# Performance work log

Measured on AMD Instinct MI355X. Metric: run time of the kernel, lower is better.

## Reference

```python
import math
import jax, jax.numpy as jnp
import numpy as np

B = 8          # number of graphs in the batch
NMAX = 256     # max nodes per graph (padding size)
K = 128        # num_kernels
H = 32         # num_heads
NTYPE = 101    # max_node_type + 1


def setup_inputs() -> dict:
    key = jax.random.key(0)
    ks = jax.random.split(key, 10)
    sizes = np.asarray(NMAX - np.arange(B) * 16, dtype=np.int32)  # 256,240,...,144 -> ragged
    N = int(sizes.sum())  # 1600
    coord = jax.random.normal(ks[0], (N, 3), dtype=jnp.float32) * 3.0
    node_type = jax.random.randint(ks[1], (N,), 0, NTYPE, dtype=jnp.int32)
    gaussian_means = jax.random.uniform(ks[2], (1, K), minval=0.0, maxval=3.0, dtype=jnp.float32)
    gaussian_stds = jax.random.uniform(ks[3], (1, K), minval=0.0, maxval=3.0, dtype=jnp.float32)
    # nn.Embedding(max_node_type+1, 2) tables; original init is const(0)/const(1),
    # we perturb so the computation is non-degenerate.
    mul_w = jax.random.normal(ks[4], (NTYPE, 2), dtype=jnp.float32) * 0.1
    bias_w = 1.0 + jax.random.normal(ks[5], (NTYPE, 2), dtype=jnp.float32) * 0.1
    W1 = jax.random.normal(ks[6], (K, K), dtype=jnp.float32) / math.sqrt(K)
    b1 = jnp.zeros((K,), dtype=jnp.float32)
    W2 = jax.random.normal(ks[7], (K, H), dtype=jnp.float32) / math.sqrt(K)
    b2 = jnp.zeros((H,), dtype=jnp.float32)
    return {
        "coord": coord,
        "gaussian_means": gaussian_means,
        "gaussian_stds": gaussian_stds,
        "mul_w": mul_w,
        "bias_w": bias_w,
        "W1": W1,
        "b1": b1,
        "W2": W2,
        "b2": b2,
        "node_type": node_type,
        "batch_num_nodes": jnp.asarray(sizes),
    }


def reference(coord, gaussian_means, gaussian_stds, mul_w, bias_w, W1, b1, W2, b2,
              node_type, batch_num_nodes):
    N = coord.shape[0]
    offsets = jnp.concatenate([jnp.zeros((1,), dtype=batch_num_nodes.dtype),
                               jnp.cumsum(batch_num_nodes)[:-1]])
    ar = jnp.arange(NMAX)
    idx = offsets[:, None] + ar[None, :]                     # [B, n] flat node index per graph slot
    valid = ar[None, :] < batch_num_nodes[:, None]           # [B, n] node mask
    idx_c = jnp.clip(idx, 0, N - 1)
    pc = coord[idx_c]                                        # [B, n, 3] padded coords
    pt = node_type[idx_c]                                    # [B, n]

    # pairwise Euclidean distance (torch.cdist p=2), sqrt-safe at 0
    diff = pc[:, :, None, :] - pc[:, None, :, :]             # [B, n, n, 3]
    sq = jnp.sum(diff * diff, axis=-1)                       # [B, n, n]
    nz = sq > 0
    dist = jnp.where(nz, jnp.sqrt(jnp.where(nz, sq, 1.0)), 0.0)

    # outer-sum of per-node (src, dst) scaling embeddings
    mul_e = mul_w[pt]                                        # [B, n, 2]
    bias_e = bias_w[pt]
    mul = mul_e[:, :, None, 0] + mul_e[:, None, :, 1]        # [B, n, n]
    bias = bias_e[:, :, None, 0] + bias_e[:, None, :, 1]
    scaled = mul * dist + bias                               # [B, n, n]

    means = gaussian_means.reshape(-1)                       # [K]
    stds = jnp.abs(gaussian_stds.reshape(-1)) + 0.01         # [K]
    z = (scaled[..., None] - means) / stds                   # [B, n, n, K]
    gk = jnp.exp(-0.5 * z * z) / (-math.sqrt(2.0 * math.pi) * stds)

    h = jax.nn.gelu(gk @ W1 + b1, approximate=False)         # exact gelu like torch F.gelu
    out = h @ W2 + b2                                        # [B, n, n, H]

    pair = valid[:, :, None] & valid[:, None, :]             # padded positions -> -inf
    return jnp.where(pair[..., None], out, -jnp.inf)
```

## Files before the change

### kernel.cpp

```cpp
#include <hip/hip_runtime.h>
#include <math.h>

#define NMAXC 256
#define KC 128
#define HC 32
#define BC 8
#define TP 256
#define NEG_SENTINEL (-1.0e30f)
#define LOG2E 1.4426950408889634f

typedef __bf16 bf16x8 __attribute__((ext_vector_type(8)));
typedef float  f32x16 __attribute__((ext_vector_type(16)));
union FragU { uint4 u; bf16x8 v; };

#if __has_builtin(__builtin_amdgcn_exp2f)
#define EXP2F(x) __builtin_amdgcn_exp2f(x)
#else
#define EXP2F(x) exp2f(x)
#endif

__device__ __forceinline__ unsigned pack2(float lo, float hi) {
    return __builtin_amdgcn_perm(__float_as_uint(hi), __float_as_uint(lo), 0x07060302u);
}

__device__ __forceinline__ int swap23(int k) {
    return (k & ~12) | ((k & 4) << 1) | ((k & 8) >> 1);
}

__global__ __launch_bounds__(256) void se3d_prep(const float* __restrict__ W1,
                                                 const float* __restrict__ W2,
                                                 const float* __restrict__ gm,
                                                 const float* __restrict__ gs,
                                                 const int* __restrict__ bnn,
                                                 unsigned* __restrict__ wsu) {
    int t = blockIdx.x * 256 + threadIdx.x;
    if (t < 2048) {
        int fb = t >> 6, lane = t & 63;
        int nt = fb >> 3, ks = fb & 7;
        int n  = nt * 32 + (lane & 31);
        int k0 = ks * 16 + 8 * (lane >> 5);
        unsigned u[4];
#pragma unroll
        for (int p = 0; p < 4; ++p)
            u[p] = pack2(-W1[(k0 + 2 * p) * KC + n], -W1[(k0 + 2 * p + 1) * KC + n]);
        ((uint4*)wsu)[t] = make_uint4(u[0], u[1], u[2], u[3]);
    } else if (t < 2560) {
        int c = t - 2048;
        int ks = c >> 6, lane = c & 63;
        int n  = lane & 31;
        int k0 = ks * 16 + 8 * (lane >> 5);
        unsigned u[4];
#pragma unroll
        for (int p = 0; p < 4; ++p) {
            int ta = swap23(k0 + 2 * p);
            int tb = swap23(k0 + 2 * p + 1);
            u[p] = pack2(W2[ta * HC + n], W2[tb * HC + n]);
        }
        ((uint4*)wsu)[2048 + c] = make_uint4(u[0], u[1], u[2], u[3]);
    } else if (t < 2688) {
        int k = t - 2560;
        float inv = 1.0f / (fabsf(gs[k]) + 0.01f);
        float m  = gm[k];
        float A2 = -0.5f * inv * inv * LOG2E;
        float* wf = (float*)wsu + 10240;
        wf[2 * k]     = A2;
        wf[2 * k + 1] = -2.0f * A2 * m;
        wf[256 + k]   = A2 * m * m + log2f(0.3989422804014327f * inv);
    } else if (t < 2696) {
        int g = t - 2688;
        int o = 0;
        for (int i = 0; i < g; ++i) o += bnn[i];
        ((int*)wsu)[10624 + g] = o;
    } else if (t < 2704) {
        int g = t - 2696;
        unsigned n = (unsigned)bnn[g];
        wsu[10632 + g] = (1u << 25) / n + 1u;
    }
}

__global__ __launch_bounds__(256, 3) void se3d_main(
    const float* __restrict__ coord, const float* __restrict__ mulw,
    const float* __restrict__ biasw, const float* __restrict__ b1,
    const float* __restrict__ b2, const int* __restrict__ ntype,
    const int* __restrict__ bnn, const void* __restrict__ ws,
    float* __restrict__ out)
{
    __shared__ __attribute__((aligned(16))) uint4 ldsW[2560];
    __shared__ float scaled[TP];
    __shared__ int   obase[TP];
    __shared__ float cAB[2 * KC];
    __shared__ float cC[KC];

    const int b = blockIdx.y;
    const int n = bnn[b];
    const int q0 = blockIdx.x * TP;
    const int tid = threadIdx.x;

    if (q0 >= n * n) {
        int v = q0 + tid - n * n;
        int wdt = 256 - n;
        int na = n * wdt;
        int i, j;
        if (v < na) { i = v / wdt; j = n + (v - i * wdt); }
        else        { int vp = v - na; i = n + (vp >> 8); j = vp & 255; }
        float4 s4 = make_float4(NEG_SENTINEL, NEG_SENTINEL, NEG_SENTINEL, NEG_SENTINEL);
        float4* o = (float4*)(out + ((size_t)((b * NMAXC + i) * NMAXC + j)) * HC);
#pragma unroll
        for (int t = 0; t < 8; ++t) o[t] = s4;
        return;
    }

    const int l = tid & 63, w = tid >> 6;

#pragma unroll
    for (int t = 0; t < 10; ++t) {
        int chunk = w * 10 + t;
        __builtin_amdgcn_global_load_lds(
            (const uint4*)ws + chunk * 64 + l,
            &ldsW[chunk * 64], 16, 0, 0);
    }

    const int      off = ((const int*)ws)[10624 + b];
    const unsigned mg  = ((const unsigned*)ws)[10632 + b];

    const float* wf = (const float*)((const char*)ws + 40960);
    cAB[tid < 256 ? tid : 0] = wf[tid < 256 ? tid : 0];
    if (tid < KC) cC[tid] = wf[256 + tid];
    {
        int q = q0 + tid;
        int i = (int)(((unsigned long long)(unsigned)q * mg) >> 25);
        int j = q - i * n;
        int gi = off + i, gj = off + j;
        float dx = coord[gi * 3 + 0] - coord[gj * 3 + 0];
        float dy = coord[gi * 3 + 1] - coord[gj * 3 + 1];
        float dz = coord[gi * 3 + 2] - coord[gj * 3 + 2];
        float sq = dx * dx + dy * dy + dz * dz;
        float dist = sq > 0.f ? sqrtf(sq) : 0.f;
        int ti = ntype[gi], tj = ntype[gj];
        scaled[tid] = (mulw[ti * 2 + 0] + mulw[tj * 2 + 1]) * dist
                    + (biasw[ti * 2 + 0] + biasw[tj * 2 + 1]);
        obase[tid]  = ((b * NMAXC + i) * NMAXC + j) * HC;
    }
    __syncthreads();

    const int hi = l >> 5, ln31 = l & 31;
    const int m0 = w * 64;
    const float sA = scaled[m0 + ln31];
    const float sB = scaled[m0 + 32 + ln31];

    const bf16x8* wsW1 = (const bf16x8*)ldsW;
    const bf16x8* wsW2 = (const bf16x8*)ldsW + 2048;

    FragU gfrA[8], gfrB[8];
#pragma unroll
    for (int ks = 0; ks < 8; ++ks) {
        int k0 = ks * 16 + 8 * hi;
        const float4* ab = (const float4*)(cAB + 2 * k0);
        const float4* cc = (const float4*)(cC + k0);
        float4 ab0 = ab[0], ab1 = ab[1], ab2 = ab[2], ab3 = ab[3];
        float4 c0 = cc[0], c1 = cc[1];
#pragma unroll
        for (int grp = 0; grp < 2; ++grp) {
            float s = grp ? sB : sA;
            float t0 = EXP2F(fmaf(fmaf(ab0.x, s, ab0.y), s, c0.x));
            float t1 = EXP2F(fmaf(fmaf(ab0.z, s, ab0.w), s, c0.y));
            float t2 = EXP2F(fmaf(fmaf(ab1.x, s, ab1.y), s, c0.z));
            float t3 = EXP2F(fmaf(fmaf(ab1.z, s, ab1.w), s, c0.w));
            float t4 = EXP2F(fmaf(fmaf(ab2.x, s, ab2.y), s, c1.x));
            float t5 = EXP2F(fmaf(fmaf(ab2.z, s, ab2.w), s, c1.y));
            float t6 = EXP2F(fmaf(fmaf(ab3.x, s, ab3.y), s, c1.z));
            float t7 = EXP2F(fmaf(fmaf(ab3.z, s, ab3.w), s, c1.w));
            FragU& g = grp ? gfrB[ks] : gfrA[ks];
            g.u.x = pack2(t0, t1);
            g.u.y = pack2(t2, t3);
            g.u.z = pack2(t4, t5);
            g.u.w = pack2(t6, t7);
        }
    }

    const float KSG = -1.702f * LOG2E;
    f32x16 c2A, c2B;
#pragma unroll
    for (int g = 0; g < 4; ++g) {
        float4 t4 = *(const float4*)(b2 + 8 * g + 4 * hi);
        c2A[4 * g + 0] = t4.x; c2A[4 * g + 1] = t4.y;
        c2A[4 * g + 2] = t4.z; c2A[4 * g + 3] = t4.w;
        c2B[4 * g + 0] = t4.x; c2B[4 * g + 1] = t4.y;
        c2B[4 * g + 2] = t4.z; c2B[4 * g + 3] = t4.w;
    }

#define GELU_PACK(AA, F0, F1) do {                                      \
    float vv[16];                                                       \
    _Pragma("unroll")                                                   \
    for (int r = 0; r < 16; ++r) {                                      \
        float x = AA[r];                                                \
        float e = EXP2F(x * KSG);                                       \
        vv[r] = x * __builtin_amdgcn_rcpf(1.0f + e);                    \
    }                                                                   \
    F0.u.x = pack2(vv[0],  vv[1]);  F0.u.y = pack2(vv[2],  vv[3]);      \
    F0.u.z = pack2(vv[4],  vv[5]);  F0.u.w = pack2(vv[6],  vv[7]);      \
    F1.u.x = pack2(vv[8],  vv[9]);  F1.u.y = pack2(vv[10], vv[11]);     \
    F1.u.z = pack2(vv[12], vv[13]); F1.u.w = pack2(vv[14], vv[15]);     \
} while (0)

#pragma unroll
    for (int nt = 0; nt < 4; ++nt) {
        f32x16 aA, aB;
#pragma unroll
        for (int g = 0; g < 4; ++g) {
            float4 t4 = *(const float4*)(b1 + nt * 32 + 8 * g + 4 * hi);
            aA[4 * g + 0] = t4.x; aA[4 * g + 1] = t4.y;
            aA[4 * g + 2] = t4.z; aA[4 * g + 3] = t4.w;
            aB[4 * g + 0] = t4.x; aB[4 * g + 1] = t4.y;
            aB[4 * g + 2] = t4.z; aB[4 * g + 3] = t4.w;
        }
#pragma unroll
        for (int ks = 0; ks < 8; ++ks) {
            bf16x8 w0 = wsW1[(nt * 8 + ks) * 64 + l];
            aA = __builtin_amdgcn_mfma_f32_32x32x16_bf16(w0, gfrA[ks].v, aA, 0, 0, 0);
            aB = __builtin_amdgcn_mfma_f32_32x32x16_bf16(w0, gfrB[ks].v, aB, 0, 0, 0);
        }
        FragU fA0, fA1, fB0, fB1;
        GELU_PACK(aA, fA0, fA1);
        GELU_PACK(aB, fB0, fB1);
        bf16x8 u0 = wsW2[(2 * nt + 0) * 64 + l];
        bf16x8 u1 = wsW2[(2 * nt + 1) * 64 + l];
        c2A = __builtin_amdgcn_mfma_f32_32x32x16_bf16(u0, fA0.v, c2A, 0, 0, 0);
        c2A = __builtin_amdgcn_mfma_f32_32x32x16_bf16(u1, fA1.v, c2A, 0, 0, 0);
        c2B = __builtin_amdgcn_mfma_f32_32x32x16_bf16(u0, fB0.v, c2B, 0, 0, 0);
        c2B = __builtin_amdgcn_mfma_f32_32x32x16_bf16(u1, fB1.v, c2B, 0, 0, 0);
    }
#undef GELU_PACK

    {
        const int obA = obase[m0 + ln31];
        float* opA = out + (size_t)obA + 4 * hi;
#pragma unroll
        for (int g = 0; g < 4; ++g)
            *(float4*)(opA + 8 * g) =
                make_float4(c2A[4 * g], c2A[4 * g + 1], c2A[4 * g + 2], c2A[4 * g + 3]);
        const int obB = obase[m0 + 32 + ln31];
        float* opB = out + (size_t)obB + 4 * hi;
#pragma unroll
        for (int g = 0; g < 4; ++g)
            *(float4*)(opB + 8 * g) =
                make_float4(c2B[4 * g], c2B[4 * g + 1], c2B[4 * g + 2], c2B[4 * g + 3]);
    }
}

extern "C" void kernel_launch(void* const* d_in, const int* in_sizes, int n_in,
                              void* d_out, int out_size, void* d_ws, size_t ws_size,
                              hipStream_t stream) {
    const float* coord = (const float*)d_in[0];
    const float* gm    = (const float*)d_in[1];
    const float* gs    = (const float*)d_in[2];
    const float* mulw  = (const float*)d_in[3];
    const float* biasw = (const float*)d_in[4];
    const float* W1    = (const float*)d_in[5];
    const float* b1    = (const float*)d_in[6];
    const float* W2    = (const float*)d_in[7];
    const float* b2    = (const float*)d_in[8];
    const int* ntype   = (const int*)d_in[9];
    const int* bnn     = (const int*)d_in[10];
    float* out = (float*)d_out;

    hipLaunchKernelGGL(se3d_prep, dim3(11), dim3(256), 0, stream,
                       W1, W2, gm, gs, bnn, (unsigned*)d_ws);
    hipLaunchKernelGGL(se3d_main, dim3(NMAXC * NMAXC / TP, BC), dim3(256),
                       0, stream,
                       coord, mulw, biasw, b1, b2, ntype, bnn, d_ws, out);
}
```

Before: 117.2 us.

## Make main kernel persistent with prefetched per-tile pair setup

```diff
diff --git a/kernel.cpp b/kernel.cpp
--- a/kernel.cpp
+++ b/kernel.cpp
@@ -6,6 +6,8 @@
 #define HC 32
 #define BC 8
 #define TP 256
+#define NTILES 2048
+#define PBLK 768
 #define NEG_SENTINEL (-1.0e30f)
 #define LOG2E 1.4426950408889634f
 
@@ -75,6 +77,8 @@
         int g = t - 2696;
         unsigned n = (unsigned)bnn[g];
         wsu[10632 + g] = (1u << 25) / n + 1u;
+    } else {
+        wsu[10640 + (t - 2704)] = 0u;
     }
 }
 
@@ -85,167 +89,193 @@
     const int* __restrict__ bnn, const void* __restrict__ ws,
     float* __restrict__ out)
 {
-    __shared__ __attribute__((aligned(16))) uint4 ldsW[2560];
-    __shared__ float scaled[TP];
-    __shared__ int   obase[TP];
-    __shared__ float cAB[2 * KC];
-    __shared__ float cC[KC];
-
-    const int b = blockIdx.y;
-    const int n = bnn[b];
-    const int q0 = blockIdx.x * TP;
+    __shared__ __attribute__((aligned(16))) uint4 ldsW[2688];
+    __shared__ float scaled[2][TP];
+    __shared__ int   obase[2][TP];
+
     const int tid = threadIdx.x;
-
-    if (q0 >= n * n) {
-        int v = q0 + tid - n * n;
-        int wdt = 256 - n;
-        int na = n * wdt;
-        int i, j;
-        if (v < na) { i = v / wdt; j = n + (v - i * wdt); }
-        else        { int vp = v - na; i = n + (vp >> 8); j = vp & 255; }
-        float4 s4 = make_float4(NEG_SENTINEL, NEG_SENTINEL, NEG_SENTINEL, NEG_SENTINEL);
-        float4* o = (float4*)(out + ((size_t)((b * NMAXC + i) * NMAXC + j)) * HC);
-#pragma unroll
-        for (int t = 0; t < 8; ++t) o[t] = s4;
-        return;
-    }
-
     const int l = tid & 63, w = tid >> 6;
-
-#pragma unroll
-    for (int t = 0; t < 10; ++t) {
-        int chunk = w * 10 + t;
-        __builtin_amdgcn_global_load_lds(
-            (const uint4*)ws + chunk * 64 + l,
-            &ldsW[chunk * 64], 16, 0, 0);
-    }
-
-    const int      off = ((const int*)ws)[10624 + b];
-    const unsigned mg  = ((const unsigned*)ws)[10632 + b];
-
-    const float* wf = (const float*)((const char*)ws + 40960);
-    cAB[tid < 256 ? tid : 0] = wf[tid < 256 ? tid : 0];
-    if (tid < KC) cC[tid] = wf[256 + tid];
-    {
-        int q = q0 + tid;
-        int i = (int)(((unsigned long long)(unsigned)q * mg) >> 25);
-        int j = q - i * n;
-        int gi = off + i, gj = off + j;
-        float dx = coord[gi * 3 + 0] - coord[gj * 3 + 0];
-        float dy = coord[gi * 3 + 1] - coord[gj * 3 + 1];
-        float dz = coord[gi * 3 + 2] - coord[gj * 3 + 2];
-        float sq = dx * dx + dy * dy + dz * dz;
-        float dist = sq > 0.f ? sqrtf(sq) : 0.f;
-        int ti = ntype[gi], tj = ntype[gj];
-        scaled[tid] = (mulw[ti * 2 + 0] + mulw[tj * 2 + 1]) * dist
-                    + (biasw[ti * 2 + 0] + biasw[tj * 2 + 1]);
-        obase[tid]  = ((b * NMAXC + i) * NMAXC + j) * HC;
-    }
-    __syncthreads();
-
     const int hi = l >> 5, ln31 = l & 31;
     const int m0 = w * 64;
-    const float sA = scaled[m0 + ln31];
-    const float sB = scaled[m0 + 32 + ln31];
-
-    const bf16x8* wsW1 = (const bf16x8*)ldsW;
-    const bf16x8* wsW2 = (const bf16x8*)ldsW + 2048;
-
-    FragU gfrA[8], gfrB[8];
-#pragma unroll
-    for (int ks = 0; ks < 8; ++ks) {
-        int k0 = ks * 16 + 8 * hi;
-        const float4* ab = (const float4*)(cAB + 2 * k0);
-        const float4* cc = (const float4*)(cC + k0);
-        float4 ab0 = ab[0], ab1 = ab[1], ab2 = ab[2], ab3 = ab[3];
-        float4 c0 = cc[0], c1 = cc[1];
-#pragma unroll
-        for (int grp = 0; grp < 2; ++grp) {
-            float s = grp ? sB : sA;
-            float t0 = EXP2F(fmaf(fmaf(ab0.x, s, ab0.y), s, c0.x));
-            float t1 = EXP2F(fmaf(fmaf(ab0.z, s, ab0.w), s, c0.y));
-            float t2 = EXP2F(fmaf(fmaf(ab1.x, s, ab1.y), s, c0.z));
-            float t3 = EXP2F(fmaf(fmaf(ab1.z, s, ab1.w), s, c0.w));
-            float t4 = EXP2F(fmaf(fmaf(ab2.x, s, ab2.y), s, c1.x));
-            float t5 = EXP2F(fmaf(fmaf(ab2.z, s, ab2.w), s, c1.y));
-            float t6 = EXP2F(fmaf(fmaf(ab3.x, s, ab3.y), s, c1.z));
-            float t7 = EXP2F(fmaf(fmaf(ab3.z, s, ab3.w), s, c1.w));
-            FragU& g = grp ? gfrB[ks] : gfrA[ks];
-            g.u.x = pack2(t0, t1);
-            g.u.y = pack2(t2, t3);
-            g.u.z = pack2(t4, t5);
-            g.u.w = pack2(t6, t7);
+
+    {
+        int nch  = 11 - (w >> 1);
+        int base = (w < 2) ? (w * 11) : (22 + (w - 2) * 10);
+        for (int t = 0; t < nch; ++t) {
+            int chunk = base + t;
+            __builtin_amdgcn_global_load_lds(
+                (const uint4*)ws + chunk * 64 + l,
+                &ldsW[chunk * 64], 16, 0, 0);
         }
     }
 
-    const float KSG = -1.702f * LOG2E;
-    f32x16 c2A, c2B;
-#pragma unroll
-    for (int g = 0; g < 4; ++g) {
-        float4 t4 = *(const float4*)(b2 + 8 * g + 4 * hi);
-        c2A[4 * g + 0] = t4.x; c2A[4 * g + 1] = t4.y;
-        c2A[4 * g + 2] = t4.z; c2A[4 * g + 3] = t4.w;
-        c2B[4 * g + 0] = t4.x; c2B[4 * g + 1] = t4.y;
-        c2B[4 * g + 2] = t4.z; c2B[4 * g + 3] = t4.w;
+#define SETUP(T, SV, OBV, TV) do {                                          \
+    int bb_ = (T) >> 8;                                                     \
+    int nn_ = bnn[bb_];                                                     \
+    int qq0_ = ((T) & 255) * TP;                                            \
+    (TV) = qq0_ < nn_ * nn_;                                                \
+    if (TV) {                                                               \
+        int off_      = ((const int*)ws)[10624 + bb_];                      \
+        unsigned mg_  = ((const unsigned*)ws)[10632 + bb_];                 \
+        int q_ = qq0_ + tid;                                                \
+        int i_ = (int)(((unsigned long long)(unsigned)q_ * mg_) >> 25);     \
+        int j_ = q_ - i_ * nn_;                                             \
+        int gi_ = off_ + i_, gj_ = off_ + j_;                               \
+        float dx_ = coord[gi_*3+0] - coord[gj_*3+0];                        \
+        float dy_ = coord[gi_*3+1] - coord[gj_*3+1];                        \
+        float dz_ = coord[gi_*3+2] - coord[gj_*3+2];                        \
+        float sq_ = dx_*dx_ + dy_*dy_ + dz_*dz_;                            \
+        float dist_ = sq_ > 0.f ? sqrtf(sq_) : 0.f;                         \
+        int ti_ = ntype[gi_], tj_ = ntype[gj_];                             \
+        (SV) = (mulw[ti_*2+0] + mulw[tj_*2+1]) * dist_                      \
+             + (biasw[ti_*2+0] + biasw[tj_*2+1]);                           \
+        (OBV) = ((bb_ * NMAXC + i_) * NMAXC + j_) * HC;                     \
+    }                                                                       \
+} while (0)
+
+    int T = blockIdx.x;
+    int cur = 0;
+    {
+        float sv; int obv; bool tv;
+        SETUP(T, sv, obv, tv);
+        if (tv) { scaled[0][tid] = sv; obase[0][tid] = obv; }
+        bool curval = tv;
+        __syncthreads();
+
+        const bf16x8* wsW1 = (const bf16x8*)ldsW;
+        const bf16x8* wsW2 = (const bf16x8*)ldsW + 2048;
+        const float*  wfAB = (const float*)ldsW + 10240;
+        const float*  wfC  = wfAB + 256;
+        const float KSG = -1.702f * LOG2E;
+
+        while (true) {
+            int Tn = T + PBLK;
+            bool have_next = Tn < NTILES;
+            float sv2; int obv2; bool tv2 = false;
+            if (have_next) SETUP(Tn, sv2, obv2, tv2);
+
+            if (!curval) {
+                int bb = T >> 8;
+                int nn = bnn[bb];
+                int qq0 = (T & 255) * TP;
+                int v = qq0 + tid - nn * nn;
+                int wdt = 256 - nn;
+                int na = nn * wdt;
+                int i, j;
+                if (v < na) { i = v / wdt; j = nn + (v - i * wdt); }
+                else        { int vp = v - na; i = nn + (vp >> 8); j = vp & 255; }
+                float4 s4 = make_float4(NEG_SENTINEL, NEG_SENTINEL,
+                                        NEG_SENTINEL, NEG_SENTINEL);
+                float4* o = (float4*)(out + ((size_t)((bb * NMAXC + i) * NMAXC + j)) * HC);
+#pragma unroll
+                for (int t = 0; t < 8; ++t) o[t] = s4;
+            } else {
+                const float sA = scaled[cur][m0 + ln31];
+                const float sB = scaled[cur][m0 + 32 + ln31];
+
+                FragU gfrA[8], gfrB[8];
+#pragma unroll
+                for (int ks = 0; ks < 8; ++ks) {
+                    int k0 = ks * 16 + 8 * hi;
+                    const float4* ab = (const float4*)(wfAB + 2 * k0);
+                    const float4* cc = (const float4*)(wfC + k0);
+                    float4 ab0 = ab[0], ab1 = ab[1], ab2 = ab[2], ab3 = ab[3];
+                    float4 c0 = cc[0], c1 = cc[1];
+#pragma unroll
+                    for (int grp = 0; grp < 2; ++grp) {
+                        float s = grp ? sB : sA;
+                        float t0 = EXP2F(fmaf(fmaf(ab0.x, s, ab0.y), s, c0.x));
+                        float t1 = EXP2F(fmaf(fmaf(ab0.z, s, ab0.w), s, c0.y));
+                        float t2 = EXP2F(fmaf(fmaf(ab1.x, s, ab1.y), s, c0.z));
+                        float t3 = EXP2F(fmaf(fmaf(ab1.z, s, ab1.w), s, c0.w));
+                        float t4 = EXP2F(fmaf(fmaf(ab2.x, s, ab2.y), s, c1.x));
+                        float t5 = EXP2F(fmaf(fmaf(ab2.z, s, ab2.w), s, c1.y));
+                        float t6 = EXP2F(fmaf(fmaf(ab3.x, s, ab3.y), s, c1.z));
+                        float t7 = EXP2F(fmaf(fmaf(ab3.z, s, ab3.w), s, c1.w));
+                        FragU& g = grp ? gfrB[ks] : gfrA[ks];
+                        g.u.x = pack2(t0, t1);
+                        g.u.y = pack2(t2, t3);
+                        g.u.z = pack2(t4, t5);
+                        g.u.w = pack2(t6, t7);
+                    }
+                }
+
+                f32x16 c2A, c2B;
+#pragma unroll
+                for (int g = 0; g < 4; ++g) {
+                    float4 t4 = *(const float4*)(b2 + 8 * g + 4 * hi);
+                    c2A[4*g+0] = t4.x; c2A[4*g+1] = t4.y;
+                    c2A[4*g+2] = t4.z; c2A[4*g+3] = t4.w;
+                    c2B[4*g+0] = t4.x; c2B[4*g+1] = t4.y;
+                    c2B[4*g+2] = t4.z; c2B[4*g+3] = t4.w;
+                }
+
+#define GELU_PACK(AA, F0, F1) do {                                          \
+    float vv[16];                                                           \
+    _Pragma("unroll")                                                       \
+    for (int r = 0; r < 16; ++r) {                                          \
+        float x = AA[r];                                                    \
+        float e = EXP2F(x * KSG);                                           \
+        vv[r] = x * __builtin_amdgcn_rcpf(1.0f + e);                        \
+    }                                                                       \
+    F0.u.x = pack2(vv[0],  vv[1]);  F0.u.y = pack2(vv[2],  vv[3]);          \
+    F0.u.z = pack2(vv[4],  vv[5]);  F0.u.w = pack2(vv[6],  vv[7]);          \
+    F1.u.x = pack2(vv[8],  vv[9]);  F1.u.y = pack2(vv[10], vv[11]);         \
+    F1.u.z = pack2(vv[12], vv[13]); F1.u.w = pack2(vv[14], vv[15]);         \
+} while (0)
+
+#pragma unroll
+                for (int nt = 0; nt < 4; ++nt) {
+                    f32x16 aA, aB;
+#pragma unroll
+                    for (int g = 0; g < 4; ++g) {
+                        float4 t4 = *(const float4*)(b1 + nt * 32 + 8 * g + 4 * hi);
+                        aA[4*g+0] = t4.x; aA[4*g+1] = t4.y;
+                        aA[4*g+2] = t4.z; aA[4*g+3] = t4.w;
+                        aB[4*g+0] = t4.x; aB[4*g+1] = t4.y;
+                        aB[4*g+2] = t4.z; aB[4*g+3] = t4.w;
+                    }
+#pragma unroll
+                    for (int ks = 0; ks < 8; ++ks) {
+                        bf16x8 w0 = wsW1[(nt * 8 + ks) * 64 + l];
+                        aA = __builtin_amdgcn_mfma_f32_32x32x16_bf16(w0, gfrA[ks].v, aA, 0, 0, 0);
+                        aB = __builtin_amdgcn_mfma_f32_32x32x16_bf16(w0, gfrB[ks].v, aB, 0, 0, 0);
+                    }
+                    FragU fA0, fA1, fB0, fB1;
+                    GELU_PACK(aA, fA0, fA1);
+                    GELU_PACK(aB, fB0, fB1);
+                    bf16x8 u0 = wsW2[(2 * nt + 0) * 64 + l];
+                    bf16x8 u1 = wsW2[(2 * nt + 1) * 64 + l];
+                    c2A = __builtin_amdgcn_mfma_f32_32x32x16_bf16(u0, fA0.v, c2A, 0, 0, 0);
+                    c2A = __builtin_amdgcn_mfma_f32_32x32x16_bf16(u1, fA1.v, c2A, 0, 0, 0);
+                    c2B = __builtin_amdgcn_mfma_f32_32x32x16_bf16(u0, fB0.v, c2B, 0, 0, 0);
+                    c2B = __builtin_amdgcn_mfma_f32_32x32x16_bf16(u1, fB1.v, c2B, 0, 0, 0);
+                }
+#undef GELU_PACK
+
+                {
+                    const int obA = obase[cur][m0 + ln31];
+                    float* opA = out + (size_t)obA + 4 * hi;
+#pragma unroll
+                    for (int g = 0; g < 4; ++g)
+                        *(float4*)(opA + 8 * g) =
+                            make_float4(c2A[4*g], c2A[4*g+1], c2A[4*g+2], c2A[4*g+3]);
+                    const int obB = obase[cur][m0 + 32 + ln31];
+                    float* opB = out + (size_t)obB + 4 * hi;
+#pragma unroll
+                    for (int g = 0; g < 4; ++g)
+                        *(float4*)(opB + 8 * g) =
+                            make_float4(c2B[4*g], c2B[4*g+1], c2B[4*g+2], c2B[4*g+3]);
+                }
+            }
+
+            if (!have_next) break;
+            if (tv2) { scaled[cur ^ 1][tid] = sv2; obase[cur ^ 1][tid] = obv2; }
+            __syncthreads();
+            cur ^= 1; T = Tn; curval = tv2;
+        }
     }
-
-#define GELU_PACK(AA, F0, F1) do {                                      \
-    float vv[16];                                                       \
-    _Pragma("unroll")                                                   \
-    for (int r = 0; r < 16; ++r) {                                      \
-        float x = AA[r];                                                \
-        float e = EXP2F(x * KSG);                                       \
-        vv[r] = x * __builtin_amdgcn_rcpf(1.0f + e);                    \
-    }                                                                   \
-    F0.u.x = pack2(vv[0],  vv[1]);  F0.u.y = pack2(vv[2],  vv[3]);      \
-    F0.u.z = pack2(vv[4],  vv[5]);  F0.u.w = pack2(vv[6],  vv[7]);      \
-    F1.u.x = pack2(vv[8],  vv[9]);  F1.u.y = pack2(vv[10], vv[11]);     \
-    F1.u.z = pack2(vv[12], vv[13]); F1.u.w = pack2(vv[14], vv[15]);     \
-} while (0)
-
-#pragma unroll
-    for (int nt = 0; nt < 4; ++nt) {
-        f32x16 aA, aB;
-#pragma unroll
-        for (int g = 0; g < 4; ++g) {
-            float4 t4 = *(const float4*)(b1 + nt * 32 + 8 * g + 4 * hi);
-            aA[4 * g + 0] = t4.x; aA[4 * g + 1] = t4.y;
-            aA[4 * g + 2] = t4.z; aA[4 * g + 3] = t4.w;
-            aB[4 * g + 0] = t4.x; aB[4 * g + 1] = t4.y;
-            aB[4 * g + 2] = t4.z; aB[4 * g + 3] = t4.w;
-        }
-#pragma unroll
-        for (int ks = 0; ks < 8; ++ks) {
-            bf16x8 w0 = wsW1[(nt * 8 + ks) * 64 + l];
-            aA = __builtin_amdgcn_mfma_f32_32x32x16_bf16(w0, gfrA[ks].v, aA, 0, 0, 0);
-            aB = __builtin_amdgcn_mfma_f32_32x32x16_bf16(w0, gfrB[ks].v, aB, 0, 0, 0);
-        }
-        FragU fA0, fA1, fB0, fB1;
-        GELU_PACK(aA, fA0, fA1);
-        GELU_PACK(aB, fB0, fB1);
-        bf16x8 u0 = wsW2[(2 * nt + 0) * 64 + l];
-        bf16x8 u1 = wsW2[(2 * nt + 1) * 64 + l];
-        c2A = __builtin_amdgcn_mfma_f32_32x32x16_bf16(u0, fA0.v, c2A, 0, 0, 0);
-        c2A = __builtin_amdgcn_mfma_f32_32x32x16_bf16(u1, fA1.v, c2A, 0, 0, 0);
-        c2B = __builtin_amdgcn_mfma_f32_32x32x16_bf16(u0, fB0.v, c2B, 0, 0, 0);
-        c2B = __builtin_amdgcn_mfma_f32_32x32x16_bf16(u1, fB1.v, c2B, 0, 0, 0);
-    }
-#undef GELU_PACK
-
-    {
-        const int obA = obase[m0 + ln31];
-        float* opA = out + (size_t)obA + 4 * hi;
-#pragma unroll
-        for (int g = 0; g < 4; ++g)
-            *(float4*)(opA + 8 * g) =
-                make_float4(c2A[4 * g], c2A[4 * g + 1], c2A[4 * g + 2], c2A[4 * g + 3]);
-        const int obB = obase[m0 + 32 + ln31];
-        float* opB = out + (size_t)obB + 4 * hi;
-#pragma unroll
-        for (int g = 0; g < 4; ++g)
-            *(float4*)(opB + 8 * g) =
-                make_float4(c2B[4 * g], c2B[4 * g + 1], c2B[4 * g + 2], c2B[4 * g + 3]);
-    }
+#undef SETUP
 }
 
 extern "C" void kernel_launch(void* const* d_in, const int* in_sizes, int n_in,
@@ -266,7 +296,6 @@
 
     hipLaunchKernelGGL(se3d_prep, dim3(11), dim3(256), 0, stream,
                        W1, W2, gm, gs, bnn, (unsigned*)d_ws);
-    hipLaunchKernelGGL(se3d_main, dim3(NMAXC * NMAXC / TP, BC), dim3(256),
-                       0, stream,
+    hipLaunchKernelGGL(se3d_main, dim3(PBLK), dim3(256), 0, stream,
                        coord, mulw, biasw, b1, b2, ntype, bnn, d_ws, out);
 }
```

New measurement: 127.0 us. 1.08x slower.
